# Optimization experiments

Measured on AMD Instinct MI355X. Metric: run time of the kernel, lower is better.

Reference implementation:

```python
import jax, jax.numpy as jnp
import numpy as np

# static config (mirrors init_kwargs)
FS = 512          # frame_seqlen
NFPB = 2          # num_frame_per_block
NIB = 3           # num image/action/state blocks
NAPB = 32         # num_action_per_block
NSPB = 1          # num_state_per_block
LOCAL = 4         # local_attn_size (frames)
FIRST = FS
IMGB = NIB * NFPB * FS
ALEN = NIB * NAPB
SLEN = NIB * NSPB
TOTAL = FIRST + IMGB + ALEN + SLEN   # 3683
DIM = 1536
NH = 12
HD = DIM // NH    # 128
EPS = 1e-6


def _build_mask():
    # faithful port of _visualize_attention_mask (the block-sparse pattern)
    m = np.zeros((TOTAL, TOTAL), dtype=bool)
    fi0, fi1 = 0, FIRST
    ib0, ib1 = fi1, fi1 + IMGB
    a0, a1 = ib1, ib1 + ALEN
    s0 = a1
    m[fi0:fi1, fi0:fi1] = True  # first image: self only (sink)
    for b in range(NIB):
        bs = ib0 + b * NFPB * FS
        be = ib0 + (b + 1) * NFPB * FS
        m[bs:be, fi0:fi1] = True                      # sink
        kv = max(ib0, be - LOCAL * FS)                # local window
        m[bs:be, kv:be] = True
        m[bs:be, a0 + b * NAPB:a0 + (b + 1) * NAPB] = True
        m[bs:be, s0 + b * NSPB:s0 + (b + 1) * NSPB] = True
    for b in range(NIB):
        ab0 = a0 + b * NAPB
        ab1 = a0 + (b + 1) * NAPB
        m[ab0:ab1, fi0:fi1] = True
        ibe = ib0 + (b + 1) * NFPB * FS
        kv = max(ib0, ibe - LOCAL * FS)
        m[ab0:ab1, kv:ibe] = True
        m[ab0:ab1, ab0:ab1] = True
        m[ab0:ab1, s0 + b * NSPB:s0 + (b + 1) * NSPB] = True
    for b in range(NIB):
        ss = s0 + b * NSPB
        se = s0 + (b + 1) * NSPB
        m[ss:se, ss:se] = True
    return m

_MASK = jnp.asarray(_build_mask())


def _rms_norm(x, g):
    # WanRMSNorm over full dim, fp32 accumulation
    v = jnp.mean(jnp.square(x.astype(jnp.float32)), axis=-1, keepdims=True)
    return (x.astype(jnp.float32) * jax.lax.rsqrt(v + EPS)).astype(x.dtype) * g


def _rope(x, cos, sin):
    # x: [B,L,n,hd]; pairs are consecutive (..., hd//2, 2)
    B, L, n, d = x.shape
    xp = x.reshape(B, L, n, d // 2, 2)
    xr, xi = xp[..., 0], xp[..., 1]
    c = cos[None, :, None, :]
    s = sin[None, :, None, :]
    yr = xr * c - xi * s
    yi = xr * s + xi * c
    return jnp.stack([yr, yi], axis=-1).reshape(B, L, n, d)


def setup_inputs() -> dict:
    key = jax.random.key(0)
    ks = jax.random.split(key, 16)
    x = jax.random.normal(ks[0], (1, TOTAL, DIM), jnp.float32)

    def mkfreq(k, L):
        ang = jax.random.uniform(k, (L, HD // 2), jnp.float32, 0.0, 2.0 * np.pi)
        return jnp.stack([jnp.cos(ang), jnp.sin(ang)], axis=-1).reshape(L, HD)

    freqs = mkfreq(ks[1], FIRST + IMGB)
    freqs_action = mkfreq(ks[2], ALEN)
    freqs_state = mkfreq(ks[3], SLEN)
    sc = 1.0 / np.sqrt(DIM)
    Wq = jax.random.normal(ks[4], (DIM, DIM), jnp.float32) * sc
    Wk = jax.random.normal(ks[5], (DIM, DIM), jnp.float32) * sc
    Wv = jax.random.normal(ks[6], (DIM, DIM), jnp.float32) * sc
    Wo = jax.random.normal(ks[7], (DIM, DIM), jnp.float32) * sc
    bq = jax.random.normal(ks[8], (DIM,), jnp.float32) * 0.01
    bk = jax.random.normal(ks[9], (DIM,), jnp.float32) * 0.01
    bv = jax.random.normal(ks[10], (DIM,), jnp.float32) * 0.01
    bo = jax.random.normal(ks[11], (DIM,), jnp.float32) * 0.01
    gq = jnp.ones((DIM,), jnp.float32)
    gk = jnp.ones((DIM,), jnp.float32)
    return {"x": x, "freqs": freqs, "freqs_action": freqs_action,
            "freqs_state": freqs_state, "Wq": Wq, "bq": bq, "Wk": Wk, "bk": bk,
            "Wv": Wv, "bv": bv, "Wo": Wo, "bo": bo, "gq": gq, "gk": gk}


def reference(x, freqs, freqs_action, freqs_state, Wq, bq, Wk, bk, Wv, bv, Wo, bo, gq, gk):
    B, L, _ = x.shape
    q = _rms_norm(x @ Wq + bq, gq).reshape(B, L, NH, HD)
    k = _rms_norm(x @ Wk + bk, gk).reshape(B, L, NH, HD)
    v = (x @ Wv + bv).reshape(B, L, NH, HD)
    # full-sequence rope: image freqs then action freqs then state freqs
    f = jnp.concatenate([freqs, freqs_action, freqs_state], axis=0).reshape(L, HD // 2, 2)
    cos, sin = f[..., 0], f[..., 1]
    q = _rope(q, cos, sin)
    k = _rope(k, cos, sin)
    scores = jnp.einsum('bqnd,bknd->bnqk', q, k) / np.sqrt(HD)
    scores = jnp.where(_MASK[None, None], scores, jnp.finfo(scores.dtype).min)
    p = jax.nn.softmax(scores, axis=-1)
    o = jnp.einsum('bnqk,bknd->bqnd', p, v).reshape(B, L, DIM)
    return o @ Wo + bo
```

## Files before the change

### kernel.cpp

```cpp
#include <hip/hip_runtime.h>

#define LSEQ 3683
#define LPAD 3840
#define DIMSZ 1536
#define NHEAD 12
#define HEADD 128
#define SM_SCALE 0.088388347648318447f

typedef unsigned short u16;
typedef unsigned int u32;
typedef __bf16 bf16x8 __attribute__((ext_vector_type(8)));
typedef float f32x4 __attribute__((ext_vector_type(4)));

__device__ __forceinline__ u16 f2b(float f) {
  u32 u = __float_as_uint(f);
  u += 0x7FFFu + ((u >> 16) & 1u);
  return (u16)(u >> 16);
}
__device__ __forceinline__ float b2f(u16 s) {
  return __uint_as_float(((u32)s) << 16);
}
__device__ __forceinline__ int imax(int a, int b) { return a > b ? a : b; }

__device__ __forceinline__ void gl_lds16(const u16* g, u16* l) {
  __builtin_amdgcn_global_load_lds((const __attribute__((address_space(1))) u32*)g,
                                   (__attribute__((address_space(3))) u32*)l,
                                   16, 0, 0);
}

__device__ __forceinline__ int xcd_swz(int orig, int nwg) {
  int q = nwg >> 3, r = nwg & 7;
  int x = orig & 7, l = orig >> 3;
  return (x < r ? x * (q + 1) : r * (q + 1) + (x - r) * q) + l;
}

#define CONV_BLOCKS 5760
__global__ void prep_kernel(const float* __restrict__ x, u16* __restrict__ xb,
                            const float* __restrict__ W0, const float* __restrict__ W1,
                            const float* __restrict__ W2, const float* __restrict__ W3,
                            u16* __restrict__ Wt) {
  __shared__ float tile[32][33];
  int bx = blockIdx.x;
  if (bx < CONV_BLOCKS) {
    long idx = (long)bx * blockDim.x + threadIdx.x;
    long base = idx * 4;
    if (base >= (long)LPAD * DIMSZ) return;
    float4 v;
    if (base < (long)LSEQ * DIMSZ) v = *(const float4*)(x + base);
    else v = make_float4(0.f, 0.f, 0.f, 0.f);
    ushort4 o;
    o.x = f2b(v.x); o.y = f2b(v.y); o.z = f2b(v.z); o.w = f2b(v.w);
    *(ushort4*)(xb + base) = o;
  } else {
    int i = bx - CONV_BLOCKS;
    int z = i / 2304;
    int r = i % 2304;
    int bxx = r % 48, byy = r / 48;
    const float* W = (z == 0) ? W0 : (z == 1) ? W1 : (z == 2) ? W2 : W3;
    u16* dst = Wt + (size_t)z * DIMSZ * DIMSZ;
    int k0 = bxx * 32, n0 = byy * 32;
    int tx = threadIdx.x & 31, ty = threadIdx.x >> 5;
    #pragma unroll
    for (int q = 0; q < 4; q++) {
      int k = k0 + ty + q * 8;
      tile[ty + q * 8][tx] = W[(size_t)k * DIMSZ + n0 + tx];
    }
    __syncthreads();
    #pragma unroll
    for (int q = 0; q < 4; q++) {
      int n = n0 + ty + q * 8;
      dst[(size_t)n * DIMSZ + k0 + tx] = f2b(tile[tx][ty + q * 8]);
    }
  }
}

#define BAR() __builtin_amdgcn_s_barrier()
#define LGK0() asm volatile("s_waitcnt lgkmcnt(0)" ::: "memory")
#define LGK8() asm volatile("s_waitcnt lgkmcnt(8)" ::: "memory")
#define VMC9() asm volatile("s_waitcnt vmcnt(9)" ::: "memory")
#define VMC6() asm volatile("s_waitcnt vmcnt(6)" ::: "memory")
#define VMC0() asm volatile("s_waitcnt vmcnt(0)" ::: "memory")
#define PRIO1() __builtin_amdgcn_s_setprio(1)
#define PRIO0() __builtin_amdgcn_s_setprio(0)

#define STG_A(buf, q, kt) \
  gl_lds16(gA + (size_t)((q) * 64) * DIMSZ + (kt), &Asg[buf][((q) * 64 + w * 8) * 64]);
#define STG_B(buf, q, kt) \
  gl_lds16(gB + (size_t)((q) * 64) * DIMSZ + (kt), &Bsg[buf][((q) * 64 + w * 8) * 64]);

#define LDA3(buf, mh) { \
  _Pragma("unroll") for (int mf = 0; mf < 3; mf++) { \
    int rb = (wm * 96 + (mh) * 48 + mf * 16) * 64; \
    Ar[mf * 2 + 0] = *(const bf16x8*)&Asg[buf][rb + off0]; \
    Ar[mf * 2 + 1] = *(const bf16x8*)&Asg[buf][rb + off1]; } }
#define LDB3(buf, nh) { \
  _Pragma("unroll") for (int nf = 0; nf < 3; nf++) { \
    int rb = (wn * 96 + (nh) * 48 + nf * 16) * 64; \
    Br[nh][nf * 2 + 0] = *(const bf16x8*)&Bsg[buf][rb + off0]; \
    Br[nh][nf * 2 + 1] = *(const bf16x8*)&Bsg[buf][rb + off1]; } }

#define MFMAQ3(mh, nh) { \
  _Pragma("unroll") for (int mf = 0; mf < 3; mf++) \
    _Pragma("unroll") for (int nf = 0; nf < 3; nf++) { \
      acc[(mh)*3+mf][(nh)*3+nf] = __builtin_amdgcn_mfma_f32_16x16x32_bf16(Ar[mf*2+0], Br[nh][nf*2+0], acc[(mh)*3+mf][(nh)*3+nf], 0, 0, 0); \
      acc[(mh)*3+mf][(nh)*3+nf] = __builtin_amdgcn_mfma_f32_16x16x32_bf16(Ar[mf*2+1], Br[nh][nf*2+1], acc[(mh)*3+mf][(nh)*3+nf], 0, 0, 0); } }

#define GEMM384_BODY() \
  STG_B(0, 0, 0) STG_B(0, 1, 0) STG_B(0, 2, 0) \
  STG_A(0, 0, 0) STG_A(0, 1, 0) STG_A(0, 2, 0) \
  STG_A(0, 3, 0) STG_A(0, 4, 0) STG_A(0, 5, 0) \
  STG_B(1, 0, 64) STG_B(1, 1, 64) STG_B(1, 2, 64) \
  STG_A(1, 0, 64) STG_A(1, 1, 64) STG_A(1, 2, 64) \
  STG_A(1, 3, 64) STG_A(1, 4, 64) STG_A(1, 5, 64) \
  VMC9(); \
  BAR(); \
  for (int i = 0; i < DIMSZ / 64 / 2 - 1; ++i) { \
    int kt2 = (2 * i + 2) * 64; \
    int kt3 = (2 * i + 3) * 64; \
    LDA3(0, 0) LDB3(0, 0) \
    LGK8(); BAR(); LGK0(); \
    PRIO1(); MFMAQ3(0, 0) PRIO0(); \
    BAR(); \
    LDB3(0, 1) \
    BAR(); LGK0(); \
    PRIO1(); MFMAQ3(0, 1) PRIO0(); \
    BAR(); \
    LDA3(0, 1) \
    STG_B(0, 0, kt2) STG_B(0, 1, kt2) STG_B(0, 2, kt2) \
    BAR(); LGK0(); \
    PRIO1(); MFMAQ3(1, 1) PRIO0(); \
    BAR(); \
    STG_A(0, 0, kt2) STG_A(0, 1, kt2) STG_A(0, 2, kt2) \
    VMC6(); BAR(); \
    PRIO1(); MFMAQ3(1, 0) PRIO0(); \
    BAR(); \
    LDA3(1, 0) LDB3(1, 0) \
    STG_A(0, 3, kt2) STG_A(0, 4, kt2) STG_A(0, 5, kt2) \
    LGK8(); BAR(); LGK0(); \
    PRIO1(); MFMAQ3(0, 0) PRIO0(); \
    BAR(); \
    LDB3(1, 1) \
    BAR(); LGK0(); \
    PRIO1(); MFMAQ3(0, 1) PRIO0(); \
    BAR(); \
    LDA3(1, 1) \
    STG_B(1, 0, kt3) STG_B(1, 1, kt3) STG_B(1, 2, kt3) \
    BAR(); LGK0(); \
    PRIO1(); MFMAQ3(1, 1) PRIO0(); \
    BAR(); \
    STG_A(1, 0, kt3) STG_A(1, 1, kt3) STG_A(1, 2, kt3) \
    STG_A(1, 3, kt3) STG_A(1, 4, kt3) STG_A(1, 5, kt3) \
    VMC9(); BAR(); \
    PRIO1(); MFMAQ3(1, 0) PRIO0(); \
    BAR(); \
  } \
  { \
    LDA3(0, 0) LDB3(0, 0) \
    LGK8(); BAR(); LGK0(); \
    PRIO1(); MFMAQ3(0, 0) PRIO0(); \
    BAR(); \
    LDB3(0, 1) \
    BAR(); LGK0(); \
    PRIO1(); MFMAQ3(0, 1) PRIO0(); \
    BAR(); \
    LDA3(0, 1) \
    BAR(); LGK0(); \
    PRIO1(); MFMAQ3(1, 1) PRIO0(); \
    BAR(); \
    VMC0(); BAR(); \
    PRIO1(); MFMAQ3(1, 0) PRIO0(); \
    BAR(); \
    LDA3(1, 0) LDB3(1, 0) \
    LGK8(); BAR(); LGK0(); \
    PRIO1(); MFMAQ3(0, 0) PRIO0(); \
    BAR(); \
    LDB3(1, 1) \
    BAR(); LGK0(); \
    PRIO1(); MFMAQ3(0, 1) PRIO0(); \
    BAR(); \
    LDA3(1, 1) \
    BAR(); LGK0(); \
    PRIO1(); MFMAQ3(1, 1) PRIO0(); \
    MFMAQ3(1, 0) \
  }

__launch_bounds__(512, 2)
__global__ void gemm_qkv384_kernel(const u16* __restrict__ A, const u16* __restrict__ Wt,
                                   const float* __restrict__ bq, const float* __restrict__ bk,
                                   const float* __restrict__ bv,
                                   u16* __restrict__ Qb, u16* __restrict__ Kb,
                                   u16* __restrict__ Vt) {
  __shared__ __align__(16) u16 Asg[2][384 * 64];
  __shared__ __align__(16) u16 Bsg[2][192 * 64];

  int wg = xcd_swz(blockIdx.x, 10 * 24);
  int nt = wg % 24;
  int m0 = (wg / 24) * 384;
  int which = nt >> 3;
  const float* bias = (which == 0) ? bq : (which == 1) ? bk : bv;

  int t = threadIdx.x;
  int lane = t & 63, w = t >> 6;
  int c = lane & 15, g = lane >> 4;
  int wm = w >> 1, wn = w & 1;

  int srow = t >> 3;
  int schunk = ((t & 7) ^ (srow & 7)) * 8;
  const u16* gA = A + (size_t)(m0 + srow) * DIMSZ + schunk;
  const u16* gB = Wt + (size_t)(nt * 192 + srow) * DIMSZ + schunk;

  int off0 = c * 64 + ((g) ^ (c & 7)) * 8;
  int off1 = c * 64 + ((g + 4) ^ (c & 7)) * 8;

  f32x4 acc[6][6];
  f32x4 zero = {0.f, 0.f, 0.f, 0.f};
  #pragma unroll
  for (int am = 0; am < 6; am++)
    #pragma unroll
    for (int an = 0; an < 6; an++) acc[am][an] = zero;
  bf16x8 Ar[6];
  bf16x8 Br[2][6];

  GEMM384_BODY()

  #pragma unroll
  for (int an = 0; an < 6; an++) {
    int ncol = (nt & 7) * 192 + wn * 96 + (an / 3) * 48 + (an % 3) * 16 + c;
    float bvv = bias[ncol];
    #pragma unroll
    for (int am = 0; am < 6; am++) {
      int rowb = m0 + wm * 96 + (am / 3) * 48 + (am % 3) * 16 + 4 * g;
      if (which == 2) {
        ushort4 pv;
        pv.x = f2b(acc[am][an][0] + bvv);
        pv.y = f2b(acc[am][an][1] + bvv);
        pv.z = f2b(acc[am][an][2] + bvv);
        pv.w = f2b(acc[am][an][3] + bvv);
        *(ushort4*)&Vt[(size_t)ncol * LPAD + rowb] = pv;
      } else {
        u16* P = (which == 1) ? Kb : Qb;
        #pragma unroll
        for (int r = 0; r < 4; r++)
          P[(size_t)(rowb + r) * DIMSZ + ncol] = f2b(acc[am][an][r] + bvv);
      }
    }
  }
}

__launch_bounds__(512, 2)
__global__ void gemm_out384_kernel(const u16* __restrict__ A, const u16* __restrict__ Bt,
                                   const float* __restrict__ bias, float* __restrict__ outF) {
  __shared__ __align__(16) u16 Asg[2][384 * 64];
  __shared__ __align__(16) u16 Bsg[2][192 * 64];

  int wg = xcd_swz(blockIdx.x, 10 * 8);
  int nt = wg % 8;
  int m0 = (wg / 8) * 384;

  int t = threadIdx.x;
  int lane = t & 63, w = t >> 6;
  int c = lane & 15, g = lane >> 4;
  int wm = w >> 1, wn = w & 1;

  int srow = t >> 3;
  int schunk = ((t & 7) ^ (srow & 7)) * 8;
  const u16* gA = A + (size_t)(m0 + srow) * DIMSZ + schunk;
  const u16* gB = Bt + (size_t)(nt * 192 + srow) * DIMSZ + schunk;

  int off0 = c * 64 + ((g) ^ (c & 7)) * 8;
  int off1 = c * 64 + ((g + 4) ^ (c & 7)) * 8;

  f32x4 acc[6][6];
  f32x4 zero = {0.f, 0.f, 0.f, 0.f};
  #pragma unroll
  for (int am = 0; am < 6; am++)
    #pragma unroll
    for (int an = 0; an < 6; an++) acc[am][an] = zero;
  bf16x8 Ar[6];
  bf16x8 Br[2][6];

  GEMM384_BODY()

  #pragma unroll
  for (int an = 0; an < 6; an++) {
    int ncol = nt * 192 + wn * 96 + (an / 3) * 48 + (an % 3) * 16 + c;
    float bvv = bias[ncol];
    #pragma unroll
    for (int am = 0; am < 6; am++) {
      int rowb = m0 + wm * 96 + (am / 3) * 48 + (am % 3) * 16 + 4 * g;
      #pragma unroll
      for (int r = 0; r < 4; r++) {
        int row = rowb + r;
        if (row < LSEQ) outF[(size_t)row * DIMSZ + ncol] = acc[am][an][r] + bvv;
      }
    }
  }
}

__launch_bounds__(256)
__global__ void normrope_kernel(u16* __restrict__ Qb, u16* __restrict__ Kb,
                                const float* __restrict__ gq, const float* __restrict__ gk,
                                const float* __restrict__ freqs, const float* __restrict__ freqs_a,
                                const float* __restrict__ freqs_s) {
  int l = blockIdx.x;
  int sel = blockIdx.y;
  u16* P = sel ? Kb : Qb;
  const float* gvec = sel ? gk : gq;
  int t = threadIdx.x;
  u16* row = P + (size_t)l * DIMSZ;
  float xv[6];
  #pragma unroll
  for (int i = 0; i < 3; i++) {
    int p = i * 256 + t;
    ushort2 u = *(const ushort2*)(row + 2 * p);
    xv[2 * i] = b2f(u.x);
    xv[2 * i + 1] = b2f(u.y);
  }
  float ss = 0.f;
  #pragma unroll
  for (int i = 0; i < 6; i++) ss += xv[i] * xv[i];
  #pragma unroll
  for (int d = 32; d; d >>= 1) ss += __shfl_down(ss, d);
  __shared__ float red[4];
  __shared__ float rshare;
  if ((t & 63) == 0) red[t >> 6] = ss;
  __syncthreads();
  if (t == 0) rshare = rsqrtf((red[0] + red[1] + red[2] + red[3]) * (1.0f / DIMSZ) + 1e-6f);
  __syncthreads();
  float rms = rshare;

  const float* f = (l < 3584) ? (freqs + (size_t)l * HEADD)
                : (l < 3680) ? (freqs_a + (size_t)(l - 3584) * HEADD)
                             : (freqs_s + (size_t)(l - 3680) * HEADD);
  #pragma unroll
  for (int i = 0; i < 3; i++) {
    int p = i * 256 + t;
    int j = p & 63;
    float2 csn = *(const float2*)(f + 2 * j);
    float2 gv = *(const float2*)(gvec + 2 * p);
    float xr = xv[2 * i] * rms * gv.x;
    float xi = xv[2 * i + 1] * rms * gv.y;
    ushort2 o;
    o.x = f2b(xr * csn.x - xi * csn.y);
    o.y = f2b(xr * csn.y + xi * csn.x);
    *(ushort2*)(row + 2 * p) = o;
  }
}

#define PSLOT_U16 16640
__launch_bounds__(256, 3)
__global__ void attn_dense_kernel(const u16* __restrict__ Q, const u16* __restrict__ K,
                                  const u16* __restrict__ Vt, u16* __restrict__ O,
                                  u16* __restrict__ DP) {
  __shared__ __align__(16) u16 Ks[2][32 * 136];
  __shared__ __align__(16) u16 Vs[2][128 * 40];
  __shared__ __align__(16) u16 Pl[4][32 * 40];

  int bx = blockIdx.x;
  int qbase, h, part, nparts, fb;
  if (bx < 48) { qbase = (bx / 12) * 128; h = bx % 12; part = 0; nparts = 1; fb = -1; }
  else if (bx < 336) { int i = bx - 48; int qb = i / 36; h = (i / 3) % 12; part = i % 3; nparts = 3; fb = 0; qbase = 512 + qb * 128; }
  else if (bx < 720) { int i = bx - 336; int qb = i / 48; h = (i / 4) % 12; part = i % 4; nparts = 4; fb = 1; qbase = 1536 + qb * 128; }
  else { int i = bx - 720; int qb = i / 48; h = (i / 4) % 12; part = i % 4; nparts = 4; fb = 2; qbase = 2560 + qb * 128; }

  int S0, E0, S1, E1, S2, E2, S3, E3, niv;
  if (fb < 0) { S0 = 0; E0 = 512; S1 = E1 = S2 = E2 = S3 = E3 = 0; niv = 1; }
  else {
    int be = 512 + (fb + 1) * 1024;
    int kv = imax(512, be - 2048);
    S0 = 0; E0 = 512; S1 = kv; E1 = be;
    S2 = 3584 + 32 * fb; E2 = S2 + 32; S3 = 3680 + fb; E3 = S3 + 1; niv = 4;
  }
  int B0 = S0 & ~31, B1 = S1 & ~31, B2 = S2 & ~31, B3 = S3 & ~31;
  int T1 = (E0 - B0 + 31) >> 5;
  int T2 = T1 + ((niv > 1) ? ((E1 - B1 + 31) >> 5) : 0);
  int T3 = T2 + ((niv > 2) ? ((E2 - B2 + 31) >> 5) : 0);
  int T4 = T3 + ((niv > 3) ? ((E3 - B3 + 31) >> 5) : 0);
  int ntile = T4;
  int rlo = (ntile * part) / nparts, rhi = (ntile * (part + 1)) / nparts;

  auto tile_of = [&](int f, int& k0, int& lo, int& hi) {
    k0 = B0 + (f << 5); lo = S0; hi = E0;
    if (niv > 1 && f >= T1) { k0 = B1 + ((f - T1) << 5); lo = S1; hi = E1; }
    if (niv > 2 && f >= T2) { k0 = B2 + ((f - T2) << 5); lo = S2; hi = E2; }
    if (niv > 3 && f >= T3) { k0 = B3 + ((f - T3) << 5); lo = S3; hi = E3; }
  };

  int T = threadIdx.x;
  int lane = T & 63, w = T >> 6, g = lane >> 4, c = lane & 15;

  const u16* kgp = K + (size_t)(T >> 3) * DIMSZ + h * HEADD + 8 * (T & 7);
  int kds = (T >> 3) * 136 + 8 * (T & 7);
  const u16* vgp = Vt + ((size_t)h * HEADD + (T >> 1)) * LPAD + 16 * (T & 1);
  int vds = (T >> 1) * 40 + 16 * (T & 1);

  uint4 sk0, sk1, sv0, sv1;
  auto stage_load = [&](int k0) {
    const u16* kp = kgp + (size_t)k0 * DIMSZ;
    sk0 = *(const uint4*)(kp);
    sk1 = *(const uint4*)(kp + 64);
    sv0 = *(const uint4*)(vgp + k0);
    sv1 = *(const uint4*)(vgp + k0 + 8);
  };
  auto stage_write = [&](int buf) {
    *(uint4*)&Ks[buf][kds] = sk0;
    *(uint4*)&Ks[buf][kds + 64] = sk1;
    *(uint4*)&Vs[buf][vds] = sv0;
    *(uint4*)&Vs[buf][vds + 8] = sv1;
  };

  int qrow0 = qbase + 32 * w;
  bf16x8 qf[2][4];
  #pragma unroll
  for (int a = 0; a < 2; a++) {
    const u16* qp = Q + (size_t)(qrow0 + a * 16 + c) * DIMSZ + h * HEADD + 8 * g;
    #pragma unroll
    for (int s = 0; s < 4; s++) qf[a][s] = *(const bf16x8*)(qp + 32 * s);
  }

  f32x4 zero = {0.f, 0.f, 0.f, 0.f};
  f32x4 acc[2][8];
  f32x4 lacc[2];
  #pragma unroll
  for (int a = 0; a < 2; a++) {
    lacc[a] = zero;
    #pragma unroll
    for (int cc = 0; cc < 8; cc++) acc[a][cc] = zero;
  }
  bf16x8 onesv;
  {
    u16 ob = 0x3F80;
    #pragma unroll
    for (int i = 0; i < 8; i++) onesv[i] = ((const __bf16*)&ob)[0];
  }

  u16* Pw = &Pl[w][0];
  __bf16* Pwh = (__bf16*)Pw;
  const float c1 = SM_SCALE * 1.44269504088896340f;
  const float c2 = 12.0f * 1.44269504088896340f;

  {
    int k0, lo, hi; tile_of(rlo, k0, lo, hi);
    stage_load(k0);
    stage_write(0);
  }
  __syncthreads();
  int cur = 0;

  for (int t = rlo; t < rhi; ++t) {
    int ck0, clo, chi; tile_of(t, ck0, clo, chi);
    bool pre = (t + 1 < rhi);
    if (pre) { int nk0, nl, nh; tile_of(t + 1, nk0, nl, nh); stage_load(nk0); }

    f32x4 sc[2][2];
    sc[0][0] = zero; sc[0][1] = zero; sc[1][0] = zero; sc[1][1] = zero;
    #pragma unroll
    for (int k2 = 0; k2 < 2; k2++)
      #pragma unroll
      for (int s = 0; s < 4; s++) {
        bf16x8 kf = *(const bf16x8*)&Ks[cur][(16 * k2 + c) * 136 + 32 * s + 8 * g];
        sc[0][k2] = __builtin_amdgcn_mfma_f32_16x16x32_bf16(qf[0][s], kf, sc[0][k2], 0, 0, 0);
        sc[1][k2] = __builtin_amdgcn_mfma_f32_16x16x32_bf16(qf[1][s], kf, sc[1][k2], 0, 0, 0);
      }

    if (ck0 >= clo && ck0 + 32 <= chi) {
      #pragma unroll
      for (int a = 0; a < 2; a++)
        #pragma unroll
        for (int k2 = 0; k2 < 2; k2++)
          #pragma unroll
          for (int r = 0; r < 4; r++) {
            float p = __builtin_amdgcn_exp2f(sc[a][k2][r] * c1 - c2);
            Pwh[(a * 16 + 4 * g + r) * 40 + k2 * 16 + c] = (__bf16)p;
          }
    } else {
      #pragma unroll
      for (int a = 0; a < 2; a++)
        #pragma unroll
        for (int k2 = 0; k2 < 2; k2++) {
          int k = ck0 + k2 * 16 + c;
          bool valid = (k >= clo) && (k < chi);
          #pragma unroll
          for (int r = 0; r < 4; r++) {
            float p = __builtin_amdgcn_exp2f(sc[a][k2][r] * c1 - c2);
            Pwh[(a * 16 + 4 * g + r) * 40 + k2 * 16 + c] = valid ? (__bf16)p : (__bf16)0.0f;
          }
        }
    }
    asm volatile("s_waitcnt lgkmcnt(0)" ::: "memory");
    __builtin_amdgcn_sched_barrier(0);

    bf16x8 pa0 = *(const bf16x8*)&Pw[c * 40 + 8 * g];
    bf16x8 pa1 = *(const bf16x8*)&Pw[(16 + c) * 40 + 8 * g];

    #pragma unroll
    for (int cc = 0; cc < 8; cc++) {
      bf16x8 vf = *(const bf16x8*)&Vs[cur][(cc * 16 + c) * 40 + 8 * g];
      acc[0][cc] = __builtin_amdgcn_mfma_f32_16x16x32_bf16(pa0, vf, acc[0][cc], 0, 0, 0);
      acc[1][cc] = __builtin_amdgcn_mfma_f32_16x16x32_bf16(pa1, vf, acc[1][cc], 0, 0, 0);
    }
    lacc[0] = __builtin_amdgcn_mfma_f32_16x16x32_bf16(pa0, onesv, lacc[0], 0, 0, 0);
    lacc[1] = __builtin_amdgcn_mfma_f32_16x16x32_bf16(pa1, onesv, lacc[1], 0, 0, 0);

    if (pre) stage_write(cur ^ 1);
    __syncthreads();
    cur ^= 1;
  }

  if (nparts == 1) {
    float inv[2][4];
    #pragma unroll
    for (int a = 0; a < 2; a++)
      #pragma unroll
      for (int r = 0; r < 4; r++) inv[a][r] = (lacc[a][r] > 0.f) ? 1.0f / lacc[a][r] : 0.f;
    #pragma unroll
    for (int a = 0; a < 2; a++)
      #pragma unroll
      for (int cc = 0; cc < 8; cc++)
        #pragma unroll
        for (int r = 0; r < 4; r++) {
          int row = qrow0 + a * 16 + 4 * g + r;
          O[(size_t)row * DIMSZ + h * HEADD + cc * 16 + c] = f2b(acc[a][cc][r] * inv[a][r]);
        }
  } else {
    int qb = (qbase - 512 - fb * 1024) >> 7;
    int sbase = (fb == 0) ? 0 : (fb == 1 ? 288 : 672);
    int slot = sbase + (qb * 12 + h) * nparts + part;
    u16* DPs = DP + (size_t)slot * PSLOT_U16;
    float* lout = (float*)(DPs + 16384);
    #pragma unroll
    for (int a = 0; a < 2; a++) {
      #pragma unroll
      for (int cc = 0; cc < 8; cc++)
        #pragma unroll
        for (int r = 0; r < 4; r++)
          DPs[(32 * w + a * 16 + 4 * g + r) * 128 + cc * 16 + c] = f2b(acc[a][cc][r]);
      if (c == 0)
        #pragma unroll
        for (int r = 0; r < 4; r++) lout[32 * w + a * 16 + 4 * g + r] = lacc[a][r];
    }
  }
}

__launch_bounds__(256)
__global__ void attn_merge_kernel(const u16* __restrict__ DP, const float* __restrict__ Part,
                                  u16* __restrict__ O) {
  int bx = blockIdx.x, h = blockIdx.y;
  int T = threadIdx.x;
  if (bx < 24) {
    int qi = bx;
    int fb = qi >> 3, qb = qi & 7;
    int nparts = (fb == 0) ? 3 : 4;
    int sbase = (fb == 0) ? 0 : (fb == 1 ? 288 : 672);
    int slot0 = sbase + (qb * 12 + h) * nparts;
    int qbase = 512 + fb * 1024 + qb * 128;
    int row = T >> 1, c0 = 64 * (T & 1);

    float sum[64];
    #pragma unroll
    for (int j = 0; j < 64; j++) sum[j] = 0.f;
    float l = 0.f;
    for (int p = 0; p < nparts; p++) {
      const u16* S = DP + (size_t)(slot0 + p) * PSLOT_U16;
      l += ((const float*)(S + 16384))[row];
      #pragma unroll
      for (int j = 0; j < 64; j += 8) {
        uint4 v = *(const uint4*)&S[row * 128 + c0 + j];
        const u16* pv = (const u16*)&v;
        #pragma unroll
        for (int q = 0; q < 8; q++) sum[j + q] += b2f(pv[q]);
      }
    }
    float inv = (l > 0.f) ? 1.0f / l : 0.f;
    u16 tmp[64];
    #pragma unroll
    for (int j = 0; j < 64; j++) tmp[j] = f2b(sum[j] * inv);
    u16* op = O + (size_t)(qbase + row) * DIMSZ + h * HEADD + c0;
    #pragma unroll
    for (int j = 0; j < 64; j += 8) *(uint4*)(op + j) = *(uint4*)&tmp[j];
  } else {
    int b = bx - 24;
    const float* A = Part + ((size_t)(b * 12 + h)) * 2 * 4160;
    const float* B = A + 4160;
    int row = T >> 3, c0 = (T & 7) * 16;
    float l = A[4096 + row] + B[4096 + row];
    float inv = (l > 0.f) ? 1.0f / l : 0.f;
    int orow = 3584 + b * 32 + row;
    u16 tmp[16];
    #pragma unroll
    for (int jj = 0; jj < 16; jj += 4) {
      float4 va = *(const float4*)&A[row * 128 + c0 + jj];
      float4 vb = *(const float4*)&B[row * 128 + c0 + jj];
      tmp[jj + 0] = f2b((va.x + vb.x) * inv);
      tmp[jj + 1] = f2b((va.y + vb.y) * inv);
      tmp[jj + 2] = f2b((va.z + vb.z) * inv);
      tmp[jj + 3] = f2b((va.w + vb.w) * inv);
    }
    u16* op = O + (size_t)orow * DIMSZ + h * HEADD + c0;
    *(uint4*)(op) = *(uint4*)&tmp[0];
    *(uint4*)(op + 8) = *(uint4*)&tmp[8];
  }
}

__launch_bounds__(256, 2)
__global__ void attn_tail_kernel(const u16* __restrict__ Q, const u16* __restrict__ K,
                                 const u16* __restrict__ Vt, u16* __restrict__ O,
                                 float* __restrict__ Part) {
  __shared__ __align__(16) char smem[20608];
  __shared__ float Lsum[32];

  int bx = blockIdx.x;
  int h = blockIdx.y;
  int qt, part;
  if (bx < 3) { qt = 112 + bx; part = 0; }
  else if (bx < 6) { qt = 112 + (bx - 3); part = 1; }
  else { qt = 115; part = 0; }
  int qbase = qt * 32;
  bool heavy = (qt <= 114);

  int t = threadIdx.x, lane = t & 63, w = t >> 6, g = lane >> 4, c = lane & 15;

  int S0, E0, S1, E1, S2, E2, S3, E3, niv;
  if (qbase < 3680) {
    int b = (qbase - 3584) >> 5;
    int ibe = 512 + (b + 1) * 1024;
    int kv = imax(512, ibe - 2048);
    S0 = 0; E0 = 512; S1 = kv; E1 = ibe;
    S2 = 3584 + 32 * b; E2 = S2 + 32; S3 = 3680 + b; E3 = S3 + 1; niv = 4;
  } else {
    S0 = 3680; E0 = 3683; S1 = S2 = S3 = 0; E1 = E2 = E3 = 0; niv = 1;
  }
  bool diag = (qbase >= 3680);

  int B0 = S0 & ~31, B1 = S1 & ~31, B2 = S2 & ~31, B3 = S3 & ~31;
  int T1 = (E0 - B0 + 31) >> 5;
  int T2 = T1 + ((niv > 1) ? ((E1 - B1 + 31) >> 5) : 0);
  int T3 = T2 + ((niv > 2) ? ((E2 - B2 + 31) >> 5) : 0);
  int T4 = T3 + ((niv > 3) ? ((E3 - B3 + 31) >> 5) : 0);
  int ntile = T4;

  int rlo = 0, rhi = ntile;
  if (heavy) { int half = (ntile + 1) >> 1; if (part == 0) rhi = half; else rlo = half; }

  auto tile_of = [&](int f, int& k0, int& lo, int& hi) {
    k0 = B0 + (f << 5); lo = S0; hi = E0;
    if (niv > 1 && f >= T1) { k0 = B1 + ((f - T1) << 5); lo = S1; hi = E1; }
    if (niv > 2 && f >= T2) { k0 = B2 + ((f - T2) << 5); lo = S2; hi = E2; }
    if (niv > 3 && f >= T3) { k0 = B3 + ((f - T3) << 5); lo = S3; hi = E3; }
  };

  bf16x8 qf[2][4];
  #pragma unroll
  for (int a = 0; a < 2; a++) {
    const u16* qp = Q + (size_t)(qbase + a * 16 + c) * DIMSZ + h * HEADD + 8 * g;
    #pragma unroll
    for (int s = 0; s < 4; s++) qf[a][s] = *(const bf16x8*)(qp + 32 * s);
  }

  f32x4 zero = {0.f, 0.f, 0.f, 0.f};
  f32x4 acc[2][8];
  f32x4 lacc[2];
  #pragma unroll
  for (int a = 0; a < 2; a++) {
    lacc[a] = zero;
    #pragma unroll
    for (int cc = 0; cc < 8; cc++) acc[a][cc] = zero;
  }
  bf16x8 onesv;
  {
    u16 ob = 0x3F80;
    #pragma unroll
    for (int i = 0; i < 8; i++) onesv[i] = ((const __bf16*)&ob)[0];
  }

  u16* PwA = (u16*)smem + w * 2560;
  u16* PwB = PwA + 1280;

  bf16x8 kc[2][4], vbuf[8], pa0, pa1;
  const float c1 = SM_SCALE * 1.44269504088896340f;
  const float c2 = 12.0f * 1.44269504088896340f;

  auto loadK = [&](int k0) {
    #pragma unroll
    for (int k2 = 0; k2 < 2; k2++) {
      const u16* kp = K + (size_t)(k0 + 16 * k2 + c) * DIMSZ + h * HEADD + 8 * g;
      #pragma unroll
      for (int s = 0; s < 4; s++) kc[k2][s] = *(const bf16x8*)(kp + 32 * s);
    }
  };
  auto loadV = [&](int k0) {
    #pragma unroll
    for (int cc = 0; cc < 8; cc++)
      vbuf[cc] = *(const bf16x8*)(Vt + (size_t)(h * HEADD + cc * 16 + c) * LPAD + k0 + 8 * g);
  };
  auto QKf = [&](f32x4 (&sc)[2][2]) {
    sc[0][0] = zero; sc[0][1] = zero; sc[1][0] = zero; sc[1][1] = zero;
    #pragma unroll
    for (int k2 = 0; k2 < 2; k2++)
      #pragma unroll
      for (int s = 0; s < 4; s++) {
        sc[0][k2] = __builtin_amdgcn_mfma_f32_16x16x32_bf16(qf[0][s], kc[k2][s], sc[0][k2], 0, 0, 0);
        sc[1][k2] = __builtin_amdgcn_mfma_f32_16x16x32_bf16(qf[1][s], kc[k2][s], sc[1][k2], 0, 0, 0);
      }
  };
  auto smstore = [&](f32x4 (&sc)[2][2], int k0, int lo, int hi, u16* Pw) {
    #pragma unroll
    for (int a = 0; a < 2; a++)
      #pragma unroll
      for (int k2 = 0; k2 < 2; k2++) {
        int k = k0 + k2 * 16 + c;
        bool valid = (k >= lo) && (k < hi);
        #pragma unroll
        for (int r = 0; r < 4; r++) {
          float p = __builtin_amdgcn_exp2f(sc[a][k2][r] * c1 - c2);
          bool v = valid;
          if (diag) { int qr = qbase + a * 16 + 4 * g + r; v = v && (k == qr); }
          Pw[(a * 16 + 4 * g + r) * 40 + k2 * 16 + c] = v ? f2b(p) : (u16)0;
        }
      }
  };
  auto readP = [&](u16* Pw) {
    pa0 = *(const bf16x8*)&Pw[c * 40 + 8 * g];
    pa1 = *(const bf16x8*)&Pw[(16 + c) * 40 + 8 * g];
  };
  auto PV = [&]() {
    #pragma unroll
    for (int cc = 0; cc < 8; cc++) {
      acc[0][cc] = __builtin_amdgcn_mfma_f32_16x16x32_bf16(pa0, vbuf[cc], acc[0][cc], 0, 0, 0);
      acc[1][cc] = __builtin_amdgcn_mfma_f32_16x16x32_bf16(pa1, vbuf[cc], acc[1][cc], 0, 0, 0);
    }
    lacc[0] = __builtin_amdgcn_mfma_f32_16x16x32_bf16(pa0, onesv, lacc[0], 0, 0, 0);
    lacc[1] = __builtin_amdgcn_mfma_f32_16x16x32_bf16(pa1, onesv, lacc[1], 0, 0, 0);
  };

  int i = rlo + w;
  if (i < rhi) {
    int ik0, ilo, ihi; tile_of(i, ik0, ilo, ihi);
    loadK(ik0);
    loadV(ik0);
    {
      f32x4 sc[2][2]; QKf(sc);
      smstore(sc, ik0, ilo, ihi, PwA);
    }
    asm volatile("s_waitcnt lgkmcnt(0)" ::: "memory");
    __builtin_amdgcn_sched_barrier(0);
    readP(PwA);
    int nx = i + 4;
    int nk0 = 0, nlo = 0, nhi = 0;
    bool useB = true;
    if (nx < rhi) { tile_of(nx, nk0, nlo, nhi); loadK(nk0); }
    while (nx < rhi) {
      int ck0 = nk0, clo = nlo, chi = nhi;
      f32x4 sc[2][2]; QKf(sc);
      int nn = nx + 4;
      if (nn < rhi) { tile_of(nn, nk0, nlo, nhi); loadK(nk0); }
      u16* Pw = useB ? PwB : PwA;
      smstore(sc, ck0, clo, chi, Pw);
      PV();
      loadV(ck0);
      asm volatile("s_waitcnt lgkmcnt(0)" ::: "memory");
      __builtin_amdgcn_sched_barrier(0);
      readP(Pw);
      useB = !useB;
      i = nx; nx = nn;
    }
    PV();
  }

  __syncthreads();
  float* Oacc = (float*)smem;
  if (w == 0) {
    #pragma unroll
    for (int a = 0; a < 2; a++) {
      #pragma unroll
      for (int cc = 0; cc < 8; cc++)
        #pragma unroll
        for (int r = 0; r < 4; r++)
          Oacc[(a * 16 + 4 * g + r) * 132 + cc * 16 + c] = acc[a][cc][r];
      if (c == 0)
        #pragma unroll
        for (int r = 0; r < 4; r++) Lsum[a * 16 + 4 * g + r] = lacc[a][r];
    }
  }
  __syncthreads();
  #pragma unroll
  for (int ww = 1; ww < 4; ww++) {
    if (w == ww) {
      #pragma unroll
      for (int a = 0; a < 2; a++) {
        #pragma unroll
        for (int cc = 0; cc < 8; cc++)
          #pragma unroll
          for (int r = 0; r < 4; r++)
            Oacc[(a * 16 + 4 * g + r) * 132 + cc * 16 + c] += acc[a][cc][r];
        if (c == 0)
          #pragma unroll
          for (int r = 0; r < 4; r++) Lsum[a * 16 + 4 * g + r] += lacc[a][r];
      }
    }
    __syncthreads();
  }

  int row = t >> 3, c0 = (t & 7) * 16;
  if (heavy) {
    size_t slot = ((size_t)((qt - 112) * 12 + h)) * 2 + part;
    float* P = Part + slot * 4160;
    #pragma unroll
    for (int j = 0; j < 16; j += 4)
      *(float4*)&P[row * 128 + c0 + j] = *(float4*)&Oacc[row * 132 + c0 + j];
    if ((t & 7) == 0) P[4096 + row] = Lsum[row];
  } else {
    int orow = qbase + row;
    if (orow < LSEQ) {
      float lsv = Lsum[row];
      float inv = (lsv > 0.f) ? 1.0f / lsv : 0.f;
      u16 tmp[16];
      #pragma unroll
      for (int j = 0; j < 16; j++) tmp[j] = f2b(Oacc[row * 132 + c0 + j] * inv);
      u16* op = O + (size_t)orow * DIMSZ + h * HEADD + c0;
      *(uint4*)(op) = *(uint4*)&tmp[0];
      *(uint4*)(op + 8) = *(uint4*)&tmp[8];
    }
  }
}

extern "C" void kernel_launch(void* const* d_in, const int* in_sizes, int n_in,
                              void* d_out, int out_size, void* d_ws, size_t ws_size,
                              hipStream_t stream) {
  (void)in_sizes; (void)n_in; (void)out_size; (void)ws_size;
  const float* x       = (const float*)d_in[0];
  const float* freqs   = (const float*)d_in[1];
  const float* freqs_a = (const float*)d_in[2];
  const float* freqs_s = (const float*)d_in[3];
  const float* Wq = (const float*)d_in[4];
  const float* bq = (const float*)d_in[5];
  const float* Wk = (const float*)d_in[6];
  const float* bk = (const float*)d_in[7];
  const float* Wv = (const float*)d_in[8];
  const float* bv = (const float*)d_in[9];
  const float* Wo = (const float*)d_in[10];
  const float* bo = (const float*)d_in[11];
  const float* gq = (const float*)d_in[12];
  const float* gk = (const float*)d_in[13];
  float* out = (float*)d_out;

  char* ws = (char*)d_ws;
  size_t off = 0;
  auto alloc = [&](size_t bytes) -> void* {
    void* p = ws + off;
    off += (bytes + 255) & ~(size_t)255;
    return p;
  };
  u16* xb   = (u16*)alloc((size_t)LPAD * DIMSZ * 2);
  u16* Wt   = (u16*)alloc((size_t)4 * DIMSZ * DIMSZ * 2);
  u16* Qb   = (u16*)alloc((size_t)LPAD * DIMSZ * 2);
  u16* Kb   = (u16*)alloc((size_t)LPAD * DIMSZ * 2);
  u16* Vt   = (u16*)alloc((size_t)DIMSZ * LPAD * 2);
  u16* Ob   = (u16*)alloc((size_t)LPAD * DIMSZ * 2);
  u16* DP   = (u16*)alloc((size_t)1056 * PSLOT_U16 * 2);
  float* PartT = (float*)alloc((size_t)3 * 12 * 2 * 4160 * 4);

  prep_kernel<<<dim3(CONV_BLOCKS + 9216), 256, 0, stream>>>(x, xb, Wq, Wk, Wv, Wo, Wt);

  gemm_qkv384_kernel<<<dim3(240), 512, 0, stream>>>(xb, Wt, bq, bk, bv, Qb, Kb, Vt);

  normrope_kernel<<<dim3(LSEQ, 2), 256, 0, stream>>>(Qb, Kb, gq, gk, freqs, freqs_a, freqs_s);

  attn_dense_kernel<<<dim3(1104), 256, 0, stream>>>(Qb, Kb, Vt, Ob, DP);
  attn_tail_kernel<<<dim3(7, 12), 256, 0, stream>>>(Qb, Kb, Vt, Ob, PartT);
  attn_merge_kernel<<<dim3(27, 12), 256, 0, stream>>>(DP, PartT, Ob);

  gemm_out384_kernel<<<dim3(80), 512, 0, stream>>>(Ob, Wt + 3 * (size_t)DIMSZ * DIMSZ, bo, out);
}
```

Measured before the change: 249.1 us.

## Restructure dense attention to in-block KV split with register-direct K/V loads

Replaces the dense attention kernel, which split KV across separate blocks and merged bf16 partials through a global workspace, with a version where each 256-thread block handles 64 query rows. Two wave pairs take alternating KV tiles and their partial outputs are reduced in shared memory. K and V are now loaded from global memory straight into registers with software prefetch, instead of being staged through LDS behind a block barrier each tile. This removes the partial-write and merge traffic, shrinking the merge kernel to the tail only, and interleaves block ids across heads. In exchange, the kernel launches fewer blocks with occupancy bound 2, and the register-direct K/V reads may be less coalesced.

```diff
diff --git a/kernel.cpp b/kernel.cpp
--- a/kernel.cpp
+++ b/kernel.cpp
@@ -347,25 +347,25 @@
   }
 }
 
-#define PSLOT_U16 16640
-__launch_bounds__(256, 3)
-__global__ void attn_dense_kernel(const u16* __restrict__ Q, const u16* __restrict__ K,
-                                  const u16* __restrict__ Vt, u16* __restrict__ O,
-                                  u16* __restrict__ DP) {
-  __shared__ __align__(16) u16 Ks[2][32 * 136];
-  __shared__ __align__(16) u16 Vs[2][128 * 40];
-  __shared__ __align__(16) u16 Pl[4][32 * 40];
-
-  int bx = blockIdx.x;
-  int qbase, h, part, nparts, fb;
-  if (bx < 48) { qbase = (bx / 12) * 128; h = bx % 12; part = 0; nparts = 1; fb = -1; }
-  else if (bx < 336) { int i = bx - 48; int qb = i / 36; h = (i / 3) % 12; part = i % 3; nparts = 3; fb = 0; qbase = 512 + qb * 128; }
-  else if (bx < 720) { int i = bx - 336; int qb = i / 48; h = (i / 4) % 12; part = i % 4; nparts = 4; fb = 1; qbase = 1536 + qb * 128; }
-  else { int i = bx - 720; int qb = i / 48; h = (i / 4) % 12; part = i % 4; nparts = 4; fb = 2; qbase = 2560 + qb * 128; }
+__launch_bounds__(256, 2)
+__global__ void attn_dense2_kernel(const u16* __restrict__ Q, const u16* __restrict__ K,
+                                   const u16* __restrict__ Vt, u16* __restrict__ O) {
+  __shared__ __align__(16) char smem[34048];
+
+  int bid = blockIdx.x;
+  int j = (bid & 7) * 84 + (bid >> 3);
+  int h = j / 56, qt = j % 56;
+  int qbase = qt * 64;
+
+  int t = threadIdx.x, lane = t & 63, w = t >> 6, g = lane >> 4, c = lane & 15;
+  int half = w & 1;
+  int kp = w >> 1;
 
   int S0, E0, S1, E1, S2, E2, S3, E3, niv;
-  if (fb < 0) { S0 = 0; E0 = 512; S1 = E1 = S2 = E2 = S3 = E3 = 0; niv = 1; }
-  else {
+  if (qbase < 512) {
+    S0 = 0; E0 = 512; S1 = E1 = S2 = E2 = S3 = E3 = 0; niv = 1;
+  } else {
+    int fb = (qbase - 512) >> 10;
     int be = 512 + (fb + 1) * 1024;
     int kv = imax(512, be - 2048);
     S0 = 0; E0 = 512; S1 = kv; E1 = be;
@@ -377,7 +377,6 @@
   int T3 = T2 + ((niv > 2) ? ((E2 - B2 + 31) >> 5) : 0);
   int T4 = T3 + ((niv > 3) ? ((E3 - B3 + 31) >> 5) : 0);
   int ntile = T4;
-  int rlo = (ntile * part) / nparts, rhi = (ntile * (part + 1)) / nparts;
 
   auto tile_of = [&](int f, int& k0, int& lo, int& hi) {
     k0 = B0 + (f << 5); lo = S0; hi = E0;
@@ -386,30 +385,7 @@
     if (niv > 3 && f >= T3) { k0 = B3 + ((f - T3) << 5); lo = S3; hi = E3; }
   };
 
-  int T = threadIdx.x;
-  int lane = T & 63, w = T >> 6, g = lane >> 4, c = lane & 15;
-
-  const u16* kgp = K + (size_t)(T >> 3) * DIMSZ + h * HEADD + 8 * (T & 7);
-  int kds = (T >> 3) * 136 + 8 * (T & 7);
-  const u16* vgp = Vt + ((size_t)h * HEADD + (T >> 1)) * LPAD + 16 * (T & 1);
-  int vds = (T >> 1) * 40 + 16 * (T & 1);
-
-  uint4 sk0, sk1, sv0, sv1;
-  auto stage_load = [&](int k0) {
-    const u16* kp = kgp + (size_t)k0 * DIMSZ;
-    sk0 = *(const uint4*)(kp);
-    sk1 = *(const uint4*)(kp + 64);
-    sv0 = *(const uint4*)(vgp + k0);
-    sv1 = *(const uint4*)(vgp + k0 + 8);
-  };
-  auto stage_write = [&](int buf) {
-    *(uint4*)&Ks[buf][kds] = sk0;
-    *(uint4*)&Ks[buf][kds + 64] = sk1;
-    *(uint4*)&Vs[buf][vds] = sv0;
-    *(uint4*)&Vs[buf][vds + 8] = sv1;
-  };
-
-  int qrow0 = qbase + 32 * w;
+  int qrow0 = qbase + 32 * half;
   bf16x8 qf[2][4];
   #pragma unroll
   for (int a = 0; a < 2; a++) {
@@ -434,36 +410,39 @@
     for (int i = 0; i < 8; i++) onesv[i] = ((const __bf16*)&ob)[0];
   }
 
-  u16* Pw = &Pl[w][0];
-  __bf16* Pwh = (__bf16*)Pw;
+  u16* PwA = (u16*)smem + w * 2560;
+  u16* PwB = PwA + 1280;
+
+  bf16x8 kc[2][4], vbuf[8], pa0, pa1;
   const float c1 = SM_SCALE * 1.44269504088896340f;
   const float c2 = 12.0f * 1.44269504088896340f;
 
-  {
-    int k0, lo, hi; tile_of(rlo, k0, lo, hi);
-    stage_load(k0);
-    stage_write(0);
-  }
-  __syncthreads();
-  int cur = 0;
-
-  for (int t = rlo; t < rhi; ++t) {
-    int ck0, clo, chi; tile_of(t, ck0, clo, chi);
-    bool pre = (t + 1 < rhi);
-    if (pre) { int nk0, nl, nh; tile_of(t + 1, nk0, nl, nh); stage_load(nk0); }
-
-    f32x4 sc[2][2];
+  auto loadK = [&](int k0) {
+    #pragma unroll
+    for (int k2 = 0; k2 < 2; k2++) {
+      const u16* kp2 = K + (size_t)(k0 + 16 * k2 + c) * DIMSZ + h * HEADD + 8 * g;
+      #pragma unroll
+      for (int s = 0; s < 4; s++) kc[k2][s] = *(const bf16x8*)(kp2 + 32 * s);
+    }
+  };
+  auto loadV = [&](int k0) {
+    #pragma unroll
+    for (int cc = 0; cc < 8; cc++)
+      vbuf[cc] = *(const bf16x8*)(Vt + (size_t)(h * HEADD + cc * 16 + c) * LPAD + k0 + 8 * g);
+  };
+  auto QKf = [&](f32x4 (&sc)[2][2]) {
     sc[0][0] = zero; sc[0][1] = zero; sc[1][0] = zero; sc[1][1] = zero;
     #pragma unroll
     for (int k2 = 0; k2 < 2; k2++)
       #pragma unroll
       for (int s = 0; s < 4; s++) {
-        bf16x8 kf = *(const bf16x8*)&Ks[cur][(16 * k2 + c) * 136 + 32 * s + 8 * g];
-        sc[0][k2] = __builtin_amdgcn_mfma_f32_16x16x32_bf16(qf[0][s], kf, sc[0][k2], 0, 0, 0);
-        sc[1][k2] = __builtin_amdgcn_mfma_f32_16x16x32_bf16(qf[1][s], kf, sc[1][k2], 0, 0, 0);
+        sc[0][k2] = __builtin_amdgcn_mfma_f32_16x16x32_bf16(qf[0][s], kc[k2][s], sc[0][k2], 0, 0, 0);
+        sc[1][k2] = __builtin_amdgcn_mfma_f32_16x16x32_bf16(qf[1][s], kc[k2][s], sc[1][k2], 0, 0, 0);
       }
-
-    if (ck0 >= clo && ck0 + 32 <= chi) {
+  };
+  auto smstore = [&](f32x4 (&sc)[2][2], int k0, int lo, int hi, u16* Pw) {
+    __bf16* Pwh = (__bf16*)Pw;
+    if (k0 >= lo && k0 + 32 <= hi) {
       #pragma unroll
       for (int a = 0; a < 2; a++)
         #pragma unroll
@@ -478,8 +457,8 @@
       for (int a = 0; a < 2; a++)
         #pragma unroll
         for (int k2 = 0; k2 < 2; k2++) {
-          int k = ck0 + k2 * 16 + c;
-          bool valid = (k >= clo) && (k < chi);
+          int k = k0 + k2 * 16 + c;
+          bool valid = (k >= lo) && (k < hi);
           #pragma unroll
           for (int r = 0; r < 4; r++) {
             float p = __builtin_amdgcn_exp2f(sc[a][k2][r] * c1 - c2);
@@ -487,119 +466,96 @@
           }
         }
     }
+  };
+  auto readP = [&](u16* Pw) {
+    pa0 = *(const bf16x8*)&Pw[c * 40 + 8 * g];
+    pa1 = *(const bf16x8*)&Pw[(16 + c) * 40 + 8 * g];
+  };
+  auto PV = [&]() {
+    #pragma unroll
+    for (int cc = 0; cc < 8; cc++) {
+      acc[0][cc] = __builtin_amdgcn_mfma_f32_16x16x32_bf16(pa0, vbuf[cc], acc[0][cc], 0, 0, 0);
+      acc[1][cc] = __builtin_amdgcn_mfma_f32_16x16x32_bf16(pa1, vbuf[cc], acc[1][cc], 0, 0, 0);
+    }
+    lacc[0] = __builtin_amdgcn_mfma_f32_16x16x32_bf16(pa0, onesv, lacc[0], 0, 0, 0);
+    lacc[1] = __builtin_amdgcn_mfma_f32_16x16x32_bf16(pa1, onesv, lacc[1], 0, 0, 0);
+  };
+
+  int i = kp;
+  if (i < ntile) {
+    int ik0, ilo, ihi; tile_of(i, ik0, ilo, ihi);
+    loadK(ik0);
+    loadV(ik0);
+    {
+      f32x4 sc[2][2]; QKf(sc);
+      smstore(sc, ik0, ilo, ihi, PwA);
+    }
     asm volatile("s_waitcnt lgkmcnt(0)" ::: "memory");
     __builtin_amdgcn_sched_barrier(0);
-
-    bf16x8 pa0 = *(const bf16x8*)&Pw[c * 40 + 8 * g];
-    bf16x8 pa1 = *(const bf16x8*)&Pw[(16 + c) * 40 + 8 * g];
-
-    #pragma unroll
-    for (int cc = 0; cc < 8; cc++) {
-      bf16x8 vf = *(const bf16x8*)&Vs[cur][(cc * 16 + c) * 40 + 8 * g];
-      acc[0][cc] = __builtin_amdgcn_mfma_f32_16x16x32_bf16(pa0, vf, acc[0][cc], 0, 0, 0);
-      acc[1][cc] = __builtin_amdgcn_mfma_f32_16x16x32_bf16(pa1, vf, acc[1][cc], 0, 0, 0);
-    }
-    lacc[0] = __builtin_amdgcn_mfma_f32_16x16x32_bf16(pa0, onesv, lacc[0], 0, 0, 0);
-    lacc[1] = __builtin_amdgcn_mfma_f32_16x16x32_bf16(pa1, onesv, lacc[1], 0, 0, 0);
-
-    if (pre) stage_write(cur ^ 1);
-    __syncthreads();
-    cur ^= 1;
-  }
-
-  if (nparts == 1) {
-    float inv[2][4];
-    #pragma unroll
-    for (int a = 0; a < 2; a++)
-      #pragma unroll
-      for (int r = 0; r < 4; r++) inv[a][r] = (lacc[a][r] > 0.f) ? 1.0f / lacc[a][r] : 0.f;
-    #pragma unroll
-    for (int a = 0; a < 2; a++)
+    readP(PwA);
+    int nx = i + 2;
+    int nk0 = 0, nlo = 0, nhi = 0;
+    bool useB = true;
+    if (nx < ntile) { tile_of(nx, nk0, nlo, nhi); loadK(nk0); }
+    while (nx < ntile) {
+      int ck0 = nk0, clo = nlo, chi = nhi;
+      f32x4 sc[2][2]; QKf(sc);
+      int nn = nx + 2;
+      if (nn < ntile) { tile_of(nn, nk0, nlo, nhi); loadK(nk0); }
+      u16* Pw = useB ? PwB : PwA;
+      smstore(sc, ck0, clo, chi, Pw);
+      PV();
+      loadV(ck0);
+      asm volatile("s_waitcnt lgkmcnt(0)" ::: "memory");
+      __builtin_amdgcn_sched_barrier(0);
+      readP(Pw);
+      useB = !useB;
+      i = nx; nx = nn;
+    }
+    PV();
+  }
+
+  __syncthreads();
+  float* Oacc = (float*)smem;
+  float* Ls = (float*)(smem + 33792);
+  if (w < 2) {
+    #pragma unroll
+    for (int a = 0; a < 2; a++) {
       #pragma unroll
       for (int cc = 0; cc < 8; cc++)
         #pragma unroll
-        for (int r = 0; r < 4; r++) {
-          int row = qrow0 + a * 16 + 4 * g + r;
-          O[(size_t)row * DIMSZ + h * HEADD + cc * 16 + c] = f2b(acc[a][cc][r] * inv[a][r]);
-        }
-  } else {
-    int qb = (qbase - 512 - fb * 1024) >> 7;
-    int sbase = (fb == 0) ? 0 : (fb == 1 ? 288 : 672);
-    int slot = sbase + (qb * 12 + h) * nparts + part;
-    u16* DPs = DP + (size_t)slot * PSLOT_U16;
-    float* lout = (float*)(DPs + 16384);
+        for (int r = 0; r < 4; r++)
+          Oacc[(half * 32 + a * 16 + 4 * g + r) * 132 + cc * 16 + c] = acc[a][cc][r];
+      if (c == 0)
+        #pragma unroll
+        for (int r = 0; r < 4; r++) Ls[half * 32 + a * 16 + 4 * g + r] = lacc[a][r];
+    }
+  }
+  __syncthreads();
+  if (w >= 2) {
     #pragma unroll
     for (int a = 0; a < 2; a++) {
       #pragma unroll
       for (int cc = 0; cc < 8; cc++)
         #pragma unroll
         for (int r = 0; r < 4; r++)
-          DPs[(32 * w + a * 16 + 4 * g + r) * 128 + cc * 16 + c] = f2b(acc[a][cc][r]);
+          Oacc[(half * 32 + a * 16 + 4 * g + r) * 132 + cc * 16 + c] += acc[a][cc][r];
       if (c == 0)
         #pragma unroll
-        for (int r = 0; r < 4; r++) lout[32 * w + a * 16 + 4 * g + r] = lacc[a][r];
-    }
-  }
-}
-
-__launch_bounds__(256)
-__global__ void attn_merge_kernel(const u16* __restrict__ DP, const float* __restrict__ Part,
-                                  u16* __restrict__ O) {
-  int bx = blockIdx.x, h = blockIdx.y;
-  int T = threadIdx.x;
-  if (bx < 24) {
-    int qi = bx;
-    int fb = qi >> 3, qb = qi & 7;
-    int nparts = (fb == 0) ? 3 : 4;
-    int sbase = (fb == 0) ? 0 : (fb == 1 ? 288 : 672);
-    int slot0 = sbase + (qb * 12 + h) * nparts;
-    int qbase = 512 + fb * 1024 + qb * 128;
-    int row = T >> 1, c0 = 64 * (T & 1);
-
-    float sum[64];
-    #pragma unroll
-    for (int j = 0; j < 64; j++) sum[j] = 0.f;
-    float l = 0.f;
-    for (int p = 0; p < nparts; p++) {
-      const u16* S = DP + (size_t)(slot0 + p) * PSLOT_U16;
-      l += ((const float*)(S + 16384))[row];
-      #pragma unroll
-      for (int j = 0; j < 64; j += 8) {
-        uint4 v = *(const uint4*)&S[row * 128 + c0 + j];
-        const u16* pv = (const u16*)&v;
-        #pragma unroll
-        for (int q = 0; q < 8; q++) sum[j + q] += b2f(pv[q]);
-      }
-    }
-    float inv = (l > 0.f) ? 1.0f / l : 0.f;
-    u16 tmp[64];
-    #pragma unroll
-    for (int j = 0; j < 64; j++) tmp[j] = f2b(sum[j] * inv);
-    u16* op = O + (size_t)(qbase + row) * DIMSZ + h * HEADD + c0;
-    #pragma unroll
-    for (int j = 0; j < 64; j += 8) *(uint4*)(op + j) = *(uint4*)&tmp[j];
-  } else {
-    int b = bx - 24;
-    const float* A = Part + ((size_t)(b * 12 + h)) * 2 * 4160;
-    const float* B = A + 4160;
-    int row = T >> 3, c0 = (T & 7) * 16;
-    float l = A[4096 + row] + B[4096 + row];
-    float inv = (l > 0.f) ? 1.0f / l : 0.f;
-    int orow = 3584 + b * 32 + row;
-    u16 tmp[16];
-    #pragma unroll
-    for (int jj = 0; jj < 16; jj += 4) {
-      float4 va = *(const float4*)&A[row * 128 + c0 + jj];
-      float4 vb = *(const float4*)&B[row * 128 + c0 + jj];
-      tmp[jj + 0] = f2b((va.x + vb.x) * inv);
-      tmp[jj + 1] = f2b((va.y + vb.y) * inv);
-      tmp[jj + 2] = f2b((va.z + vb.z) * inv);
-      tmp[jj + 3] = f2b((va.w + vb.w) * inv);
-    }
-    u16* op = O + (size_t)orow * DIMSZ + h * HEADD + c0;
-    *(uint4*)(op) = *(uint4*)&tmp[0];
-    *(uint4*)(op + 8) = *(uint4*)&tmp[8];
-  }
+        for (int r = 0; r < 4; r++) Ls[half * 32 + a * 16 + 4 * g + r] += lacc[a][r];
+    }
+  }
+  __syncthreads();
+
+  int row = t >> 2, c0 = (t & 3) * 32;
+  float l = Ls[row];
+  float inv = (l > 0.f) ? 1.0f / l : 0.f;
+  u16 tmp[32];
+  #pragma unroll
+  for (int jj = 0; jj < 32; jj++) tmp[jj] = f2b(Oacc[row * 132 + c0 + jj] * inv);
+  u16* op = O + (size_t)(qbase + row) * DIMSZ + h * HEADD + c0;
+  #pragma unroll
+  for (int jj = 0; jj < 32; jj += 8) *(uint4*)(op + jj) = *(uint4*)&tmp[jj];
 }
 
 __launch_bounds__(256, 2)
@@ -824,6 +780,31 @@
   }
 }
 
+__launch_bounds__(256)
+__global__ void attn_merge_tail(const float* __restrict__ Part, u16* __restrict__ O) {
+  int b = blockIdx.x, h = blockIdx.y;
+  const float* A = Part + ((size_t)(b * 12 + h)) * 2 * 4160;
+  const float* B = A + 4160;
+  int t = threadIdx.x;
+  int row = t >> 3, c0 = (t & 7) * 16;
+  float l = A[4096 + row] + B[4096 + row];
+  float inv = (l > 0.f) ? 1.0f / l : 0.f;
+  int orow = 3584 + b * 32 + row;
+  u16 tmp[16];
+  #pragma unroll
+  for (int jj = 0; jj < 16; jj += 4) {
+    float4 va = *(const float4*)&A[row * 128 + c0 + jj];
+    float4 vb = *(const float4*)&B[row * 128 + c0 + jj];
+    tmp[jj + 0] = f2b((va.x + vb.x) * inv);
+    tmp[jj + 1] = f2b((va.y + vb.y) * inv);
+    tmp[jj + 2] = f2b((va.z + vb.z) * inv);
+    tmp[jj + 3] = f2b((va.w + vb.w) * inv);
+  }
+  u16* op = O + (size_t)orow * DIMSZ + h * HEADD + c0;
+  *(uint4*)(op) = *(uint4*)&tmp[0];
+  *(uint4*)(op + 8) = *(uint4*)&tmp[8];
+}
+
 extern "C" void kernel_launch(void* const* d_in, const int* in_sizes, int n_in,
                               void* d_out, int out_size, void* d_ws, size_t ws_size,
                               hipStream_t stream) {
@@ -857,7 +838,6 @@
   u16* Kb   = (u16*)alloc((size_t)LPAD * DIMSZ * 2);
   u16* Vt   = (u16*)alloc((size_t)DIMSZ * LPAD * 2);
   u16* Ob   = (u16*)alloc((size_t)LPAD * DIMSZ * 2);
-  u16* DP   = (u16*)alloc((size_t)1056 * PSLOT_U16 * 2);
   float* PartT = (float*)alloc((size_t)3 * 12 * 2 * 4160 * 4);
 
   prep_kernel<<<dim3(CONV_BLOCKS + 9216), 256, 0, stream>>>(x, xb, Wq, Wk, Wv, Wo, Wt);
@@ -866,9 +846,9 @@
 
   normrope_kernel<<<dim3(LSEQ, 2), 256, 0, stream>>>(Qb, Kb, gq, gk, freqs, freqs_a, freqs_s);
 
-  attn_dense_kernel<<<dim3(1104), 256, 0, stream>>>(Qb, Kb, Vt, Ob, DP);
+  attn_dense2_kernel<<<dim3(672), 256, 0, stream>>>(Qb, Kb, Vt, Ob);
   attn_tail_kernel<<<dim3(7, 12), 256, 0, stream>>>(Qb, Kb, Vt, Ob, PartT);
-  attn_merge_kernel<<<dim3(27, 12), 256, 0, stream>>>(DP, PartT, Ob);
+  attn_merge_tail<<<dim3(3, 12), 256, 0, stream>>>(PartT, Ob);
 
   gemm_out384_kernel<<<dim3(80), 512, 0, stream>>>(Ob, Wt + 3 * (size_t)DIMSZ * DIMSZ, bo, out);
 }
```

Measured after the change: 405.1 us. +62.6%, slower.
